# Kernel tuning notes

Measured on AMD Instinct MI355X. Metric: run time of the kernel, lower is better.

Reference implementation:

```python
import jax, jax.numpy as jnp
import numpy as np

D = 256      # d_model
NH = 8       # num_heads
NP = 4       # n_points
H = 100      # feature map height (single level)
W = 100      # feature map width
B = 4
Q = H * W
S = H * W


def setup_inputs() -> dict:
    key = jax.random.key(0)
    ks = jax.random.split(key, 12)
    p = lambda k, shp, s=0.02: jax.random.normal(k, shp, jnp.float32) * s
    return {
        "hidden_states": jax.random.normal(ks[0], (B, Q, D), jnp.float32),
        "encoder_hidden_states": jax.random.normal(ks[1], (B, S, D), jnp.float32),
        "reference_points": jax.random.uniform(ks[2], (B, Q, 1, 2), jnp.float32),
        "spatial_shapes": jnp.array([[H, W]], dtype=jnp.int32),
        "W_off": p(ks[3], (NH * NP * 2, D)),
        "b_off": p(ks[4], (NH * NP * 2,), 0.5),
        "W_attn": p(ks[5], (NH * NP, D)),
        "b_attn": jnp.zeros((NH * NP,), jnp.float32),
        "W_val": p(ks[6], (D, D)),
        "b_val": jnp.zeros((D,), jnp.float32),
        "W_out": p(ks[7], (D, D)),
        "b_out": jnp.zeros((D,), jnp.float32),
    }


def _deform_attn(hidden_states, encoder_hidden_states, reference_points,
                 W_off, b_off, W_attn, b_attn, W_val, b_val, W_out, b_out):
    Bsz, Qn, Dm = hidden_states.shape
    d = Dm // NH

    # value projection -> [B, NH, S, d]
    value = (encoder_hidden_states @ W_val.T + b_val).reshape(Bsz, S, NH, d)
    vflat = value.transpose(0, 2, 1, 3).reshape(Bsz * NH, H * W, d)

    # sampling offsets [B,Q,NH,NP,2] (n_levels=1 squeezed)
    off = (hidden_states @ W_off.T + b_off).reshape(Bsz, Qn, NH, NP, 2)
    # attention weights softmax over (n_levels*n_points)=NP -> [B,Q,NH,NP]
    attn = jax.nn.softmax((hidden_states @ W_attn.T + b_attn).reshape(Bsz, Qn, NH, NP), axis=-1)

    # normalized sampling locations: ref + off / [W, H]
    normalizer = jnp.array([W, H], jnp.float32)
    # reference_points: [B,Q,1,2] (level dim) -> broadcast over heads/points
    loc = reference_points[:, :, None, 0, None, :] + off / normalizer  # [B,Q,NH,NP,2]

    # grid_sample semantics: grid = 2*loc - 1, align_corners=False, zeros padding
    gx = 2.0 * loc[..., 0] - 1.0
    gy = 2.0 * loc[..., 1] - 1.0
    x = ((gx + 1.0) * W - 1.0) * 0.5   # pixel coords [B,Q,NH,NP]
    y = ((gy + 1.0) * H - 1.0) * 0.5
    x0 = jnp.floor(x); y0 = jnp.floor(y)
    x1 = x0 + 1.0;     y1 = y0 + 1.0
    wx1 = x - x0; wx0 = 1.0 - wx1
    wy1 = y - y0; wy0 = 1.0 - wy1

    bh = jnp.arange(Bsz * NH)[:, None]

    def corner(xi, yi, wgt):
        valid = (xi >= 0) & (xi <= W - 1) & (yi >= 0) & (yi <= H - 1)
        xi_c = jnp.clip(xi, 0, W - 1).astype(jnp.int32)
        yi_c = jnp.clip(yi, 0, H - 1).astype(jnp.int32)
        idx = (yi_c * W + xi_c).transpose(0, 2, 1, 3).reshape(Bsz * NH, Qn * NP)
        g = vflat[bh, idx]  # [B*NH, Q*NP, d]
        wv = (wgt * valid.astype(wgt.dtype)).transpose(0, 2, 1, 3).reshape(Bsz * NH, Qn * NP, 1)
        return g * wv

    sampled = corner(x0, y0, wx0 * wy0)
    sampled = sampled + corner(x1, y0, wx1 * wy0)
    sampled = sampled + corner(x0, y1, wx0 * wy1)
    sampled = sampled + corner(x1, y1, wx1 * wy1)
    sampled = sampled.reshape(Bsz, NH, Qn, NP, d)

    out = jnp.einsum("bhqpd,bqhp->bqhd", sampled, attn).reshape(Bsz, Qn, Dm)
    return out @ W_out.T + b_out


def reference(hidden_states, encoder_hidden_states, reference_points, spatial_shapes,
              W_off, b_off, W_attn, b_attn, W_val, b_val, W_out, b_out):
    # spatial_shapes is static metadata (must equal [[H, W]]); shapes are baked in.
    return _deform_attn(hidden_states, encoder_hidden_states, reference_points,
                        W_off, b_off, W_attn, b_attn, W_val, b_val, W_out, b_out)
```

## Files before the change

kernel.cpp:

```cpp
#include <hip/hip_runtime.h>

constexpr int HH = 100;
constexpr int WW = 100;
constexpr int NH = 8;
constexpr int NP = 4;
constexpr int B  = 4;
constexpr int Q  = HH * WW;
constexpr int S  = Q;
constexpr int K  = 256;
constexpr int DH = 32;
constexpr int M  = B * Q;
constexpr int NTILES = M / 32;

typedef __attribute__((ext_vector_type(8))) short short8;
typedef __attribute__((ext_vector_type(4))) float f32x4;

__device__ inline unsigned short f2bf(float f) {
    unsigned u = __builtin_bit_cast(unsigned, f);
    u += 0x7fffu + ((u >> 16) & 1u);
    return (unsigned short)(u >> 16);
}
__device__ inline float bf2f(unsigned short h) {
    return __builtin_bit_cast(float, ((unsigned)h) << 16);
}
__device__ inline unsigned short f2h(float f) {
    _Float16 h = (_Float16)f;
    return __builtin_bit_cast(unsigned short, h);
}
__device__ inline float h2f(unsigned short u) {
    return (float)__builtin_bit_cast(_Float16, u);
}

__device__ inline void lds_st16s(short* base, int row, int stride, int kcol, short8 v) {
    *reinterpret_cast<short8*>(&base[row * stride + (kcol ^ ((row & 7) << 3))]) = v;
}
__device__ inline short8 lds_ld16s(const short* base, int row, int stride, int kcol) {
    return *reinterpret_cast<const short8*>(&base[row * stride + (kcol ^ ((row & 7) << 3))]);
}

__device__ inline short8 cvt8(float4 a, float4 b) {
    short8 r;
    r[0] = (short)f2bf(a.x); r[1] = (short)f2bf(a.y);
    r[2] = (short)f2bf(a.z); r[3] = (short)f2bf(a.w);
    r[4] = (short)f2bf(b.x); r[5] = (short)f2bf(b.y);
    r[6] = (short)f2bf(b.z); r[7] = (short)f2bf(b.w);
    return r;
}

__global__ __launch_bounds__(1024) void stage1(
    const float* __restrict__ enc, const float* __restrict__ Wval,
    const float* __restrict__ bval, unsigned short* __restrict__ vflat,
    const float* __restrict__ hidden, const float* __restrict__ Woff,
    const float* __restrict__ Wattn, const float* __restrict__ boff,
    const float* __restrict__ battn, unsigned short* __restrict__ proj)
{
    __shared__ __align__(16) short As[2][32 * 256];

    const int tid  = threadIdx.x;
    const int lane = tid & 63, w = tid >> 6;
    const int l15  = lane & 15, l4 = lane >> 4;
    const int arow = tid >> 5, ak = (tid & 31) * 8;

    constexpr int NV = 143, NJ = 113;

    if (blockIdx.x < NV) {
        const int n = w * 16 + l15;
        short8 breg[8];
#pragma unroll
        for (int ks = 0; ks < 8; ++ks) {
            const float* s = &Wval[(size_t)n * K + ks * 32 + l4 * 8];
            breg[ks] = cvt8(*reinterpret_cast<const float4*>(s),
                            *reinterpret_cast<const float4*>(s + 4));
        }
        const float bv = bval[n];
        const int h = n >> 5, dd = n & 31;

        int t = blockIdx.x;
        float4 fa0, fa1;
        auto lda = [&](int tt) {
            const float* s = &enc[(size_t)(tt * 32 + arow) * K + ak];
            fa0 = *reinterpret_cast<const float4*>(s);
            fa1 = *reinterpret_cast<const float4*>(s + 4);
        };
        lda(t);
        lds_st16s(As[0], arow, 256, ak, cvt8(fa0, fa1));
        __syncthreads();
        int cur = 0;
        for (; t < NTILES; t += NV) {
            const bool more = (t + NV < NTILES);
            if (more) lda(t + NV);

            f32x4 acc0 = {0.f, 0.f, 0.f, 0.f}, acc1 = {0.f, 0.f, 0.f, 0.f};
#pragma unroll
            for (int ks = 0; ks < 8; ++ks) {
                const int kc = ks * 32 + l4 * 8;
                const short8 a0 = lds_ld16s(As[cur], l15, 256, kc);
                const short8 a1 = lds_ld16s(As[cur], 16 + l15, 256, kc);
                acc0 = __builtin_amdgcn_mfma_f32_16x16x32_bf16(a0, breg[ks], acc0, 0, 0, 0);
                acc1 = __builtin_amdgcn_mfma_f32_16x16x32_bf16(a1, breg[ks], acc1, 0, 0, 0);
            }
            const int m0 = t * 32;
#pragma unroll
            for (int r = 0; r < 4; ++r) {
                int m = m0 + l4 * 4 + r;
                int b_ = m / S, s_ = m - b_ * S;
                vflat[(((size_t)(b_ * NH + h)) * S + s_) * DH + dd] = f2bf(acc0[r] + bv);
                m += 16; b_ = m / S; s_ = m - b_ * S;
                vflat[(((size_t)(b_ * NH + h)) * S + s_) * DH + dd] = f2bf(acc1[r] + bv);
            }
            if (more) lds_st16s(As[cur ^ 1], arow, 256, ak, cvt8(fa0, fa1));
            __syncthreads();
            cur ^= 1;
        }
    } else {
        const int nf = w >> 1, mh = w & 1;
        const int n = nf * 16 + l15;
        short8 breg[8];
        float bv = 0.f;
        if (w < 12) {
#pragma unroll
            for (int ks = 0; ks < 8; ++ks) {
                const float* s = (n < 64)
                    ? &Woff[(size_t)n * K + ks * 32 + l4 * 8]
                    : &Wattn[(size_t)(n - 64) * K + ks * 32 + l4 * 8];
                breg[ks] = cvt8(*reinterpret_cast<const float4*>(s),
                                *reinterpret_cast<const float4*>(s + 4));
            }
            bv = (n < 64) ? boff[n] : battn[n - 64];
        }

        int t = blockIdx.x - NV;
        float4 fa0, fa1;
        auto lda = [&](int tt) {
            const float* s = &hidden[(size_t)(tt * 32 + arow) * K + ak];
            fa0 = *reinterpret_cast<const float4*>(s);
            fa1 = *reinterpret_cast<const float4*>(s + 4);
        };
        lda(t);
        lds_st16s(As[0], arow, 256, ak, cvt8(fa0, fa1));
        __syncthreads();
        int cur = 0;
        for (; t < NTILES; t += NJ) {
            const bool more = (t + NJ < NTILES);
            if (more) lda(t + NJ);

            if (w < 12) {
                f32x4 acc = {0.f, 0.f, 0.f, 0.f};
#pragma unroll
                for (int ks = 0; ks < 8; ++ks) {
                    const int kc = ks * 32 + l4 * 8;
                    const short8 a = lds_ld16s(As[cur], mh * 16 + l15, 256, kc);
                    acc = __builtin_amdgcn_mfma_f32_16x16x32_bf16(a, breg[ks], acc, 0, 0, 0);
                }
#pragma unroll
                for (int r = 0; r < 4; ++r) {
                    const int m = t * 32 + mh * 16 + l4 * 4 + r;
                    proj[(size_t)m * 96 + n] = f2h(acc[r] + bv);
                }
            }
            if (more) lds_st16s(As[cur ^ 1], arow, 256, ak, cvt8(fa0, fa1));
            __syncthreads();
            cur ^= 1;
        }
    }
}

__global__ __launch_bounds__(256) void sample_agg(
    const unsigned short* __restrict__ vflat,
    const unsigned short* __restrict__ proj,
    const float* __restrict__ ref,
    unsigned short* __restrict__ tmp)
{
    const int nblk = gridDim.x;
    const int cpx  = nblk >> 3;
    const int swz  = (blockIdx.x & 7) * cpx + (blockIdx.x >> 3);

    const int lg   = threadIdx.x >> 2;
    const int lane = threadIdx.x & 3;
    const int d0   = lane * 8;

    const int g  = swz * 64 + lg;
    const int q  = g % Q;
    const int bh = g / Q;
    const int b  = bh >> 3;
    const int h  = bh & 7;

    const size_t bq = (size_t)b * Q + q;
    const float refx = ref[bq * 2 + 0];
    const float refy = ref[bq * 2 + 1];
    const unsigned short* pr = proj + bq * 96;

    float l[NP];
#pragma unroll
    for (int p = 0; p < NP; ++p) l[p] = h2f(pr[64 + h * 4 + p]);
    const float mx = fmaxf(fmaxf(l[0], l[1]), fmaxf(l[2], l[3]));
    float e[NP];
    float esum = 0.f;
#pragma unroll
    for (int p = 0; p < NP; ++p) { e[p] = __expf(l[p] - mx); esum += e[p]; }
    const float inv = 1.f / esum;

    const unsigned short* vbase = vflat + (size_t)bh * (S * DH);

    int   cidx[NP][4];
    float cw[NP][4];
#pragma unroll
    for (int p = 0; p < NP; ++p) {
        const float ox = h2f(pr[h * 8 + p * 2 + 0]);
        const float oy = h2f(pr[h * 8 + p * 2 + 1]);
        const float x = fmaf(refx, (float)WW, ox) - 0.5f;
        const float y = fmaf(refy, (float)HH, oy) - 0.5f;
        const float x0f = floorf(x), y0f = floorf(y);
        const float wx1 = x - x0f, wx0 = 1.f - wx1;
        const float wy1 = y - y0f, wy0 = 1.f - wy1;
        const int x0 = (int)x0f, y0 = (int)y0f;
        const bool vx0 = (x0 >= 0) && (x0 < WW);
        const bool vx1 = (x0 + 1 >= 0) && (x0 + 1 < WW);
        const bool vy0 = (y0 >= 0) && (y0 < HH);
        const bool vy1 = (y0 + 1 >= 0) && (y0 + 1 < HH);
        const int xi0 = min(max(x0, 0), WW - 1);
        const int xi1 = min(max(x0 + 1, 0), WW - 1);
        const int yi0 = min(max(y0, 0), HH - 1);
        const int yi1 = min(max(y0 + 1, 0), HH - 1);
        const float ap = e[p] * inv;
        cw[p][0] = ap * wx0 * wy0 * ((vx0 && vy0) ? 1.f : 0.f);
        cw[p][1] = ap * wx1 * wy0 * ((vx1 && vy0) ? 1.f : 0.f);
        cw[p][2] = ap * wx0 * wy1 * ((vx0 && vy1) ? 1.f : 0.f);
        cw[p][3] = ap * wx1 * wy1 * ((vx1 && vy1) ? 1.f : 0.f);
        cidx[p][0] = (yi0 * WW + xi0) * DH + d0;
        cidx[p][1] = (yi0 * WW + xi1) * DH + d0;
        cidx[p][2] = (yi1 * WW + xi0) * DH + d0;
        cidx[p][3] = (yi1 * WW + xi1) * DH + d0;
    }

    float o[8];
#pragma unroll
    for (int j = 0; j < 8; ++j) o[j] = 0.f;
#pragma unroll
    for (int p = 0; p < NP; ++p) {
#pragma unroll
        for (int c = 0; c < 4; ++c) {
            const short8 v = *reinterpret_cast<const short8*>(&vbase[cidx[p][c]]);
            const float wgt = cw[p][c];
#pragma unroll
            for (int j = 0; j < 8; ++j)
                o[j] = fmaf(wgt, bf2f((unsigned short)v[j]), o[j]);
        }
    }

    short8 ov;
#pragma unroll
    for (int j = 0; j < 8; ++j) ov[j] = (short)f2bf(o[j]);
    *reinterpret_cast<short8*>(&tmp[bq * 256 + h * 32 + d0]) = ov;
}

__global__ __launch_bounds__(1024) void out_proj(
    const unsigned short* __restrict__ tmp, const float* __restrict__ Wo,
    const float* __restrict__ bo, float* __restrict__ out)
{
    __shared__ __align__(16) short As[2][32 * 256];

    const int tid  = threadIdx.x;
    const int lane = tid & 63, w = tid >> 6;
    const int l15  = lane & 15, l4 = lane >> 4;
    const int arow = tid >> 5, ak = (tid & 31) * 8;

    const int n = w * 16 + l15;
    short8 breg[8];
#pragma unroll
    for (int ks = 0; ks < 8; ++ks) {
        const float* s = &Wo[(size_t)n * K + ks * 32 + l4 * 8];
        breg[ks] = cvt8(*reinterpret_cast<const float4*>(s),
                        *reinterpret_cast<const float4*>(s + 4));
    }
    const float bv = bo[n];

    int t = blockIdx.x;
    short8 sa;
    auto lda = [&](int tt) {
        sa = *reinterpret_cast<const short8*>(&tmp[(size_t)(tt * 32 + arow) * K + ak]);
    };
    lda(t);
    lds_st16s(As[0], arow, 256, ak, sa);
    __syncthreads();
    int cur = 0;
    for (; t < NTILES; t += 256) {
        const bool more = (t + 256 < NTILES);
        if (more) lda(t + 256);

        f32x4 acc0 = {0.f, 0.f, 0.f, 0.f}, acc1 = {0.f, 0.f, 0.f, 0.f};
#pragma unroll
        for (int ks = 0; ks < 8; ++ks) {
            const int kc = ks * 32 + l4 * 8;
            const short8 a0 = lds_ld16s(As[cur], l15, 256, kc);
            const short8 a1 = lds_ld16s(As[cur], 16 + l15, 256, kc);
            acc0 = __builtin_amdgcn_mfma_f32_16x16x32_bf16(a0, breg[ks], acc0, 0, 0, 0);
            acc1 = __builtin_amdgcn_mfma_f32_16x16x32_bf16(a1, breg[ks], acc1, 0, 0, 0);
        }
        const int m0 = t * 32;
#pragma unroll
        for (int r = 0; r < 4; ++r) {
            const int m = m0 + l4 * 4 + r;
            out[(size_t)m * K + n] = acc0[r] + bv;
            out[(size_t)(m + 16) * K + n] = acc1[r] + bv;
        }
        if (more) lds_st16s(As[cur ^ 1], arow, 256, ak, sa);
        __syncthreads();
        cur ^= 1;
    }
}

extern "C" void kernel_launch(void* const* d_in, const int* in_sizes, int n_in,
                              void* d_out, int out_size, void* d_ws, size_t ws_size,
                              hipStream_t stream)
{
    const float* hidden = (const float*)d_in[0];
    const float* enc    = (const float*)d_in[1];
    const float* refp   = (const float*)d_in[2];
    const float* W_off  = (const float*)d_in[4];
    const float* b_off  = (const float*)d_in[5];
    const float* W_attn = (const float*)d_in[6];
    const float* b_attn = (const float*)d_in[7];
    const float* W_val  = (const float*)d_in[8];
    const float* b_val  = (const float*)d_in[9];
    const float* W_out  = (const float*)d_in[10];
    const float* b_out  = (const float*)d_in[11];
    float* out = (float*)d_out;

    unsigned short* vflat = (unsigned short*)d_ws;
    unsigned short* proj  = vflat + (size_t)10240000;
    unsigned short* tmp   = proj + (size_t)3840000;

    stage1<<<256, 1024, 0, stream>>>(
        enc, W_val, b_val, vflat, hidden, W_off, W_attn, b_off, b_attn, proj);

    sample_agg<<<5000, 256, 0, stream>>>(vflat, proj, refp, tmp);

    out_proj<<<256, 1024, 0, stream>>>(tmp, W_out, b_out, out);
}
```

Before: 72.97 us.

## Swap MFMA operands to store contiguous output vectors in projection GEMMs

The three GEMM phases (value projection, offset/attention projection, output projection) now pass weights as the A operand and activations as the B operand of the MFMA. Each lane's accumulator then holds 4 consecutive output columns of one row, which lets the epilogue write packed 8-byte bf16/fp16 or 16-byte fp32 vectors instead of scattered 2- or 4-byte stores. Warps are regrouped so each covers 32 columns and 16 rows, which halves LDS A-fragment loads per MFMA pair but doubles the weight registers held per lane. The offset/attention branch now uses 6 active warps instead of 12.

```diff
diff --git a/kernel.cpp b/kernel.cpp
--- a/kernel.cpp
+++ b/kernel.cpp
@@ -15,6 +15,8 @@
 typedef __attribute__((ext_vector_type(8))) short short8;
 typedef __attribute__((ext_vector_type(4))) float f32x4;
 
+struct __align__(8) ushort4p { unsigned short x, y, z, w; };
+
 __device__ inline unsigned short f2bf(float f) {
     unsigned u = __builtin_bit_cast(unsigned, f);
     u += 0x7fffu + ((u >> 16) & 1u);
@@ -64,16 +66,24 @@
     constexpr int NV = 143, NJ = 113;
 
     if (blockIdx.x < NV) {
-        const int n = w * 16 + l15;
-        short8 breg[8];
-#pragma unroll
-        for (int ks = 0; ks < 8; ++ks) {
-            const float* s = &Wval[(size_t)n * K + ks * 32 + l4 * 8];
-            breg[ks] = cvt8(*reinterpret_cast<const float4*>(s),
-                            *reinterpret_cast<const float4*>(s + 4));
-        }
-        const float bv = bval[n];
-        const int h = n >> 5, dd = n & 31;
+        const int mg = w >> 3;
+        const int ng = w & 7;
+        short8 breg[2][8];
+#pragma unroll
+        for (int j = 0; j < 2; ++j) {
+            const int row = ng * 32 + j * 16 + l15;
+#pragma unroll
+            for (int ks = 0; ks < 8; ++ks) {
+                const float* s = &Wval[(size_t)row * K + ks * 32 + l4 * 8];
+                breg[j][ks] = cvt8(*reinterpret_cast<const float4*>(s),
+                                   *reinterpret_cast<const float4*>(s + 4));
+            }
+        }
+        const int n00 = ng * 32 + l4 * 4;
+        const int n01 = n00 + 16;
+        const float4 b40 = *reinterpret_cast<const float4*>(&bval[n00]);
+        const float4 b41 = *reinterpret_cast<const float4*>(&bval[n01]);
+        const int dd00 = n00 & 31, dd01 = n01 & 31;
 
         int t = blockIdx.x;
         float4 fa0, fa1;
@@ -93,40 +103,57 @@
             f32x4 acc0 = {0.f, 0.f, 0.f, 0.f}, acc1 = {0.f, 0.f, 0.f, 0.f};
 #pragma unroll
             for (int ks = 0; ks < 8; ++ks) {
-                const int kc = ks * 32 + l4 * 8;
-                const short8 a0 = lds_ld16s(As[cur], l15, 256, kc);
-                const short8 a1 = lds_ld16s(As[cur], 16 + l15, 256, kc);
-                acc0 = __builtin_amdgcn_mfma_f32_16x16x32_bf16(a0, breg[ks], acc0, 0, 0, 0);
-                acc1 = __builtin_amdgcn_mfma_f32_16x16x32_bf16(a1, breg[ks], acc1, 0, 0, 0);
-            }
-            const int m0 = t * 32;
-#pragma unroll
-            for (int r = 0; r < 4; ++r) {
-                int m = m0 + l4 * 4 + r;
-                int b_ = m / S, s_ = m - b_ * S;
-                vflat[(((size_t)(b_ * NH + h)) * S + s_) * DH + dd] = f2bf(acc0[r] + bv);
-                m += 16; b_ = m / S; s_ = m - b_ * S;
-                vflat[(((size_t)(b_ * NH + h)) * S + s_) * DH + dd] = f2bf(acc1[r] + bv);
+                const short8 a = lds_ld16s(As[cur], mg * 16 + l15, 256, ks * 32 + l4 * 8);
+                acc0 = __builtin_amdgcn_mfma_f32_16x16x32_bf16(breg[0][ks], a, acc0, 0, 0, 0);
+                acc1 = __builtin_amdgcn_mfma_f32_16x16x32_bf16(breg[1][ks], a, acc1, 0, 0, 0);
+            }
+            const int m = t * 32 + mg * 16 + l15;
+            const int b_ = m / S, s_ = m - b_ * S;
+            const size_t obase = (((size_t)(b_ * NH + ng)) * S + s_) * DH;
+            {
+                ushort4p pk;
+                pk.x = f2bf(acc0[0] + b40.x);
+                pk.y = f2bf(acc0[1] + b40.y);
+                pk.z = f2bf(acc0[2] + b40.z);
+                pk.w = f2bf(acc0[3] + b40.w);
+                *reinterpret_cast<ushort4p*>(&vflat[obase + dd00]) = pk;
+            }
+            {
+                ushort4p pk;
+                pk.x = f2bf(acc1[0] + b41.x);
+                pk.y = f2bf(acc1[1] + b41.y);
+                pk.z = f2bf(acc1[2] + b41.z);
+                pk.w = f2bf(acc1[3] + b41.w);
+                *reinterpret_cast<ushort4p*>(&vflat[obase + dd01]) = pk;
             }
             if (more) lds_st16s(As[cur ^ 1], arow, 256, ak, cvt8(fa0, fa1));
             __syncthreads();
             cur ^= 1;
         }
     } else {
-        const int nf = w >> 1, mh = w & 1;
-        const int n = nf * 16 + l15;
-        short8 breg[8];
-        float bv = 0.f;
-        if (w < 12) {
-#pragma unroll
-            for (int ks = 0; ks < 8; ++ks) {
-                const float* s = (n < 64)
-                    ? &Woff[(size_t)n * K + ks * 32 + l4 * 8]
-                    : &Wattn[(size_t)(n - 64) * K + ks * 32 + l4 * 8];
-                breg[ks] = cvt8(*reinterpret_cast<const float4*>(s),
-                                *reinterpret_cast<const float4*>(s + 4));
-            }
-            bv = (n < 64) ? boff[n] : battn[n - 64];
+        const int ng = w >> 1, mg = w & 1;
+        short8 breg[2][8];
+        float4 b40 = {0.f, 0.f, 0.f, 0.f}, b41 = {0.f, 0.f, 0.f, 0.f};
+        int n00 = 0, n01 = 0;
+        if (w < 6) {
+#pragma unroll
+            for (int j = 0; j < 2; ++j) {
+                const int row = ng * 32 + j * 16 + l15;
+#pragma unroll
+                for (int ks = 0; ks < 8; ++ks) {
+                    const float* s = (row < 64)
+                        ? &Woff[(size_t)row * K + ks * 32 + l4 * 8]
+                        : &Wattn[(size_t)(row - 64) * K + ks * 32 + l4 * 8];
+                    breg[j][ks] = cvt8(*reinterpret_cast<const float4*>(s),
+                                       *reinterpret_cast<const float4*>(s + 4));
+                }
+            }
+            n00 = ng * 32 + l4 * 4;
+            n01 = n00 + 16;
+            b40 = (n00 < 64) ? *reinterpret_cast<const float4*>(&boff[n00])
+                             : *reinterpret_cast<const float4*>(&battn[n00 - 64]);
+            b41 = (n01 < 64) ? *reinterpret_cast<const float4*>(&boff[n01])
+                             : *reinterpret_cast<const float4*>(&battn[n01 - 64]);
         }
 
         int t = blockIdx.x - NV;
@@ -144,18 +171,30 @@
             const bool more = (t + NJ < NTILES);
             if (more) lda(t + NJ);
 
-            if (w < 12) {
-                f32x4 acc = {0.f, 0.f, 0.f, 0.f};
+            if (w < 6) {
+                f32x4 acc0 = {0.f, 0.f, 0.f, 0.f}, acc1 = {0.f, 0.f, 0.f, 0.f};
 #pragma unroll
                 for (int ks = 0; ks < 8; ++ks) {
-                    const int kc = ks * 32 + l4 * 8;
-                    const short8 a = lds_ld16s(As[cur], mh * 16 + l15, 256, kc);
-                    acc = __builtin_amdgcn_mfma_f32_16x16x32_bf16(a, breg[ks], acc, 0, 0, 0);
+                    const short8 a = lds_ld16s(As[cur], mg * 16 + l15, 256, ks * 32 + l4 * 8);
+                    acc0 = __builtin_amdgcn_mfma_f32_16x16x32_bf16(breg[0][ks], a, acc0, 0, 0, 0);
+                    acc1 = __builtin_amdgcn_mfma_f32_16x16x32_bf16(breg[1][ks], a, acc1, 0, 0, 0);
                 }
-#pragma unroll
-                for (int r = 0; r < 4; ++r) {
-                    const int m = t * 32 + mh * 16 + l4 * 4 + r;
-                    proj[(size_t)m * 96 + n] = f2h(acc[r] + bv);
+                const int m = t * 32 + mg * 16 + l15;
+                {
+                    ushort4p pk;
+                    pk.x = f2h(acc0[0] + b40.x);
+                    pk.y = f2h(acc0[1] + b40.y);
+                    pk.z = f2h(acc0[2] + b40.z);
+                    pk.w = f2h(acc0[3] + b40.w);
+                    *reinterpret_cast<ushort4p*>(&proj[(size_t)m * 96 + n00]) = pk;
+                }
+                {
+                    ushort4p pk;
+                    pk.x = f2h(acc1[0] + b41.x);
+                    pk.y = f2h(acc1[1] + b41.y);
+                    pk.z = f2h(acc1[2] + b41.z);
+                    pk.w = f2h(acc1[3] + b41.w);
+                    *reinterpret_cast<ushort4p*>(&proj[(size_t)m * 96 + n01]) = pk;
                 }
             }
             if (more) lds_st16s(As[cur ^ 1], arow, 256, ak, cvt8(fa0, fa1));
@@ -265,15 +304,23 @@
     const int l15  = lane & 15, l4 = lane >> 4;
     const int arow = tid >> 5, ak = (tid & 31) * 8;
 
-    const int n = w * 16 + l15;
-    short8 breg[8];
-#pragma unroll
-    for (int ks = 0; ks < 8; ++ks) {
-        const float* s = &Wo[(size_t)n * K + ks * 32 + l4 * 8];
-        breg[ks] = cvt8(*reinterpret_cast<const float4*>(s),
-                        *reinterpret_cast<const float4*>(s + 4));
-    }
-    const float bv = bo[n];
+    const int mg = w >> 3;
+    const int ng = w & 7;
+    short8 breg[2][8];
+#pragma unroll
+    for (int j = 0; j < 2; ++j) {
+        const int row = ng * 32 + j * 16 + l15;
+#pragma unroll
+        for (int ks = 0; ks < 8; ++ks) {
+            const float* s = &Wo[(size_t)row * K + ks * 32 + l4 * 8];
+            breg[j][ks] = cvt8(*reinterpret_cast<const float4*>(s),
+                               *reinterpret_cast<const float4*>(s + 4));
+        }
+    }
+    const int n00 = ng * 32 + l4 * 4;
+    const int n01 = n00 + 16;
+    const float4 b40 = *reinterpret_cast<const float4*>(&bo[n00]);
+    const float4 b41 = *reinterpret_cast<const float4*>(&bo[n01]);
 
     int t = blockIdx.x;
     short8 sa;
@@ -291,18 +338,22 @@
         f32x4 acc0 = {0.f, 0.f, 0.f, 0.f}, acc1 = {0.f, 0.f, 0.f, 0.f};
 #pragma unroll
         for (int ks = 0; ks < 8; ++ks) {
-            const int kc = ks * 32 + l4 * 8;
-            const short8 a0 = lds_ld16s(As[cur], l15, 256, kc);
-            const short8 a1 = lds_ld16s(As[cur], 16 + l15, 256, kc);
-            acc0 = __builtin_amdgcn_mfma_f32_16x16x32_bf16(a0, breg[ks], acc0, 0, 0, 0);
-            acc1 = __builtin_amdgcn_mfma_f32_16x16x32_bf16(a1, breg[ks], acc1, 0, 0, 0);
-        }
-        const int m0 = t * 32;
-#pragma unroll
-        for (int r = 0; r < 4; ++r) {
-            const int m = m0 + l4 * 4 + r;
-            out[(size_t)m * K + n] = acc0[r] + bv;
-            out[(size_t)(m + 16) * K + n] = acc1[r] + bv;
+            const short8 a = lds_ld16s(As[cur], mg * 16 + l15, 256, ks * 32 + l4 * 8);
+            acc0 = __builtin_amdgcn_mfma_f32_16x16x32_bf16(breg[0][ks], a, acc0, 0, 0, 0);
+            acc1 = __builtin_amdgcn_mfma_f32_16x16x32_bf16(breg[1][ks], a, acc1, 0, 0, 0);
+        }
+        const int m = t * 32 + mg * 16 + l15;
+        {
+            float4 pv;
+            pv.x = acc0[0] + b40.x; pv.y = acc0[1] + b40.y;
+            pv.z = acc0[2] + b40.z; pv.w = acc0[3] + b40.w;
+            *reinterpret_cast<float4*>(&out[(size_t)m * K + n00]) = pv;
+        }
+        {
+            float4 pv;
+            pv.x = acc1[0] + b41.x; pv.y = acc1[1] + b41.y;
+            pv.z = acc1[2] + b41.z; pv.w = acc1[3] + b41.w;
+            *reinterpret_cast<float4*>(&out[(size_t)m * K + n01]) = pv;
         }
         if (more) lds_st16s(As[cur ^ 1], arow, 256, ak, sa);
         __syncthreads();
```

Measured after the change: 92.63 us. 1.27x slower.
